# Optimization experiments

Hardware: AMD Instinct MI355X
Metric: run time of the kernel (lower is better)

Reference implementation:

```python
import jax, jax.numpy as jnp
import numpy as np

B, T, D, E, H, F, K = 4, 2048, 2048, 16, 1024, 1024, 2


def setup_inputs() -> dict:
    key = jax.random.key(0)
    ks = jax.random.split(key, 7)
    sD, sH, sF = D ** -0.5, H ** -0.5, F ** -0.5
    hidden_state = jax.random.normal(ks[0], (B, T, D), jnp.float32)
    Wr = jax.random.normal(ks[1], (D, E), jnp.float32) * sD      # router
    Wg = jax.random.normal(ks[2], (D, 1), jnp.float32) * sD      # shared gate
    W1 = jax.random.normal(ks[3], (E, D, H), jnp.float32) * sD   # expert up-proj
    W2 = jax.random.normal(ks[4], (E, H, D), jnp.float32) * sH   # expert down-proj
    W1s = jax.random.normal(ks[5], (D, F), jnp.float32) * sD     # shared expert up
    W2s = jax.random.normal(ks[6], (F, D), jnp.float32) * sF     # shared expert down
    return {"hidden_state": hidden_state, "Wr": Wr, "Wg": Wg,
            "W1": W1, "W2": W2, "W1s": W1s, "W2s": W2s}


def reference(hidden_state, Wr, Wg, W1, W2, W1s, W2s):
    b, t, d = hidden_state.shape
    N = b * t
    x = hidden_state.reshape(N, d)

    # Router: softmax scores + shared-expert sigmoid gate
    s = jax.nn.softmax(x @ Wr, axis=-1)           # [N, E]
    g_shared = jax.nn.sigmoid(x @ Wg)             # [N, 1]

    topk_vals, topk_idx = jax.lax.top_k(s, K)     # [N, K]

    # Dense combine weights: gate[n,e] = topk_vals if expert e chosen, else 0.
    # Mathematically identical to sort/gather/scatter-add dispatch in the source.
    gate = jnp.zeros((N, E), dtype=s.dtype).at[
        jnp.arange(N)[:, None], topk_idx].add(topk_vals)

    # Per-expert FFN (fixed small expert loop), gate-weighted combine
    y = jnp.zeros_like(x)
    for e in range(E):
        h = jax.nn.gelu(x @ W1[e], approximate=False)   # [N, H]
        y = y + gate[:, e:e + 1] * (h @ W2[e])

    # Shared expert, scaled by sigmoid gate
    shared = jax.nn.gelu(x @ W1s, approximate=False) @ W2s
    y = y + g_shared * shared
    y_out = y.reshape(b, t, d)

    # Aux stats (attention_mask is None branch)
    importance = s.mean(axis=0)                               # [E]
    counts = jnp.zeros((E,), jnp.float32).at[topk_idx.reshape(-1)].add(1.0)
    load = counts / (counts.sum() + 1e-12)
    return y_out, importance, load
```

## Files before the change

kernel.cpp:

```cpp
#include <hip/hip_runtime.h>
#include <hip/hip_bf16.h>


#define N_TOK 8192
#define DDIM  2048
#define NEXP  16
#define HDIM  1024
#define FDIM  1024
#define NASSIGN (N_TOK * 2)
#define NROWS (NASSIGN + N_TOK)

typedef __attribute__((ext_vector_type(8))) short bf16x8;
typedef __attribute__((ext_vector_type(4))) float f32x4;
typedef __attribute__((ext_vector_type(8))) unsigned short u16x8;
typedef __attribute__((ext_vector_type(4))) unsigned short u16x4;

__device__ inline unsigned short f2bf(float f) {
    unsigned int u = __builtin_bit_cast(unsigned int, f);
    u += 0x7FFFu + ((u >> 16) & 1u);
    return (unsigned short)(u >> 16);
}

__device__ inline float bf2f(unsigned short h) {
    return __builtin_bit_cast(float, (unsigned int)h << 16);
}

__device__ inline float gelu_f(float v) {
    return 0.5f * v * (1.0f + erff(v * 0.7071067811865475f));
}

__device__ inline void gld16(void* lds, const void* g) {
    __builtin_amdgcn_global_load_lds(
        (const __attribute__((address_space(1))) unsigned int*)g,
        (__attribute__((address_space(3))) unsigned int*)lds, 16, 0, 0);
}

__global__ __launch_bounds__(256) void zero_small(float* imp) {
    if (threadIdx.x < NEXP) imp[threadIdx.x] = 0.0f;
}

__global__ __launch_bounds__(256) void cast_x_kernel(const float* __restrict__ x,
                                                     unsigned short* __restrict__ xb) {
    size_t i = (size_t)blockIdx.x * 256 + threadIdx.x;
    const float4 a = ((const float4*)x)[i * 2];
    const float4 b = ((const float4*)x)[i * 2 + 1];
    u16x8 o;
    o[0] = f2bf(a.x); o[1] = f2bf(a.y); o[2] = f2bf(a.z); o[3] = f2bf(a.w);
    o[4] = f2bf(b.x); o[5] = f2bf(b.y); o[6] = f2bf(b.z); o[7] = f2bf(b.w);
    *(u16x8*)(xb + i * 8) = o;
}

template <int R, int C>
__global__ __launch_bounds__(256) void transpose_cast(const float* __restrict__ src,
                                                      unsigned short* __restrict__ dst) {
    __shared__ unsigned short t[64][66];
    const size_t zoff = (size_t)blockIdx.z * R * C;
    src += zoff; dst += zoff;
    const int r0 = blockIdx.y * 64, c0 = blockIdx.x * 64;
    const int tid = threadIdx.x;
    const int cr = tid >> 4;
    const int cc4 = (tid & 15) * 4;
#pragma unroll
    for (int it = 0; it < 4; ++it) {
        int row = cr + it * 16;
        const float4 v = *(const float4*)(src + (size_t)(r0 + row) * C + c0 + cc4);
        t[row][cc4 + 0] = f2bf(v.x); t[row][cc4 + 1] = f2bf(v.y);
        t[row][cc4 + 2] = f2bf(v.z); t[row][cc4 + 3] = f2bf(v.w);
    }
    __syncthreads();
#pragma unroll
    for (int it = 0; it < 4; ++it) {
        int cc = cr + it * 16;
        u16x4 o;
#pragma unroll
        for (int j = 0; j < 4; ++j) o[j] = t[cc4 + j][cc];
        *(u16x4*)(dst + (size_t)(c0 + cc) * R + r0 + cc4) = o;
    }
}

__global__ __launch_bounds__(256) void router_kernel(
    const float* __restrict__ x, const float* __restrict__ Wr, const float* __restrict__ Wg,
    float* __restrict__ gsh, int* __restrict__ t2i, float* __restrict__ t2v,
    float* __restrict__ imp) {
    __shared__ float simp[NEXP];
    const int tid = threadIdx.x, lane = tid & 63, w = tid >> 6;
    if (tid < NEXP) simp[tid] = 0.0f;
    __syncthreads();
    const int n = blockIdx.x * 4 + w;
    const float* xr = x + (size_t)n * DDIM;
    float acc[NEXP];
#pragma unroll
    for (int e = 0; e < NEXP; ++e) acc[e] = 0.0f;
    float ag = 0.0f;
    for (int j = 0; j < DDIM / 64; ++j) {
        int d = lane + j * 64;
        float xv = xr[d];
        const float* wr = Wr + (size_t)d * NEXP;
#pragma unroll
        for (int e = 0; e < NEXP; ++e) acc[e] = fmaf(xv, wr[e], acc[e]);
        ag = fmaf(xv, Wg[d], ag);
    }
#pragma unroll
    for (int off = 32; off; off >>= 1) {
#pragma unroll
        for (int e = 0; e < NEXP; ++e) acc[e] += __shfl_xor(acc[e], off);
        ag += __shfl_xor(ag, off);
    }
    if (lane == 0) {
        float mx = acc[0];
#pragma unroll
        for (int e = 1; e < NEXP; ++e) mx = fmaxf(mx, acc[e]);
        float p[NEXP], s = 0.0f;
#pragma unroll
        for (int e = 0; e < NEXP; ++e) { p[e] = expf(acc[e] - mx); s += p[e]; }
        const float inv = 1.0f / s;
        int i1 = 0; float v1 = -1.0f;
#pragma unroll
        for (int e = 0; e < NEXP; ++e) {
            p[e] *= inv;
            if (p[e] > v1) { v1 = p[e]; i1 = e; }
        }
        int i2 = 0; float v2 = -1.0f;
#pragma unroll
        for (int e = 0; e < NEXP; ++e) {
            if (e != i1 && p[e] > v2) { v2 = p[e]; i2 = e; }
        }
        t2i[2 * n] = i1; t2i[2 * n + 1] = i2;
        t2v[2 * n] = v1; t2v[2 * n + 1] = v2;
        gsh[n] = 1.0f / (1.0f + expf(-ag));
#pragma unroll
        for (int e = 0; e < NEXP; ++e) atomicAdd(&simp[e], p[e]);
    }
    __syncthreads();
    if (tid < NEXP) unsafeAtomicAdd(&imp[tid], simp[tid]);
}

__global__ __launch_bounds__(256) void scan_finalize(
    const int* __restrict__ t2i, const float* __restrict__ imp,
    int* __restrict__ offs, int* __restrict__ fill, float* __restrict__ out_tail) {
    __shared__ int hist[NEXP];
    const int tid = threadIdx.x;
    if (tid < NEXP) hist[tid] = 0;
    __syncthreads();
    for (int i = tid; i < NASSIGN; i += 256) atomicAdd(&hist[t2i[i]], 1);
    __syncthreads();
    if (tid == 0) {
        int o = 0;
        for (int e = 0; e < NEXP; ++e) { offs[e] = o; o += hist[e]; }
        offs[NEXP] = o;
        offs[NEXP + 1] = NROWS;
    }
    if (tid < NEXP) {
        fill[tid] = 0;
        out_tail[tid] = imp[tid] * (1.0f / (float)N_TOK);
        out_tail[NEXP + tid] = (float)hist[tid] / (float)NASSIGN;
    }
}

__global__ __launch_bounds__(256) void build_assign(
    const int* __restrict__ t2i, const float* __restrict__ t2v,
    const int* __restrict__ offs, int* __restrict__ fill,
    int* __restrict__ atok, float* __restrict__ agate, int* __restrict__ t2pos) {
    const int n = blockIdx.x * 256 + threadIdx.x;
#pragma unroll
    for (int k = 0; k < 2; ++k) {
        int e = t2i[2 * n + k];
        int pos = offs[e] + atomicAdd(&fill[e], 1);
        atok[pos] = n;
        agate[pos] = t2v[2 * n + k];
        t2pos[2 * n + k] = pos;
    }
    atok[NASSIGN + n] = n;
    agate[NASSIGN + n] = 1.0f;
}

__global__ __launch_bounds__(256) void combine_kernel(
    const unsigned short* __restrict__ contrib, const int* __restrict__ t2pos,
    const float* __restrict__ gsh, float* __restrict__ y) {
    const int gi = blockIdx.x * 256 + threadIdx.x;
    const int n = gi >> 8;
    const int d8 = (gi & 255) * 8;
    const int p0 = t2pos[2 * n], p1 = t2pos[2 * n + 1];
    const float g = gsh[n];
    u16x8 a = *(const u16x8*)(contrib + (size_t)p0 * DDIM + d8);
    u16x8 b = *(const u16x8*)(contrib + (size_t)p1 * DDIM + d8);
    u16x8 c = *(const u16x8*)(contrib + (size_t)(NASSIGN + n) * DDIM + d8);
    float4 y0, y1;
    y0.x = bf2f(a[0]) + bf2f(b[0]) + g * bf2f(c[0]);
    y0.y = bf2f(a[1]) + bf2f(b[1]) + g * bf2f(c[1]);
    y0.z = bf2f(a[2]) + bf2f(b[2]) + g * bf2f(c[2]);
    y0.w = bf2f(a[3]) + bf2f(b[3]) + g * bf2f(c[3]);
    y1.x = bf2f(a[4]) + bf2f(b[4]) + g * bf2f(c[4]);
    y1.y = bf2f(a[5]) + bf2f(b[5]) + g * bf2f(c[5]);
    y1.z = bf2f(a[6]) + bf2f(b[6]) + g * bf2f(c[6]);
    y1.w = bf2f(a[7]) + bf2f(b[7]) + g * bf2f(c[7]);
    float* yr = y + (size_t)n * DDIM + d8;
    *(float4*)yr = y0;
    *(float4*)(yr + 4) = y1;
}

template <int MODE>
__global__ __launch_bounds__(512, 2) void gemm2p(
    const unsigned short* __restrict__ A, const unsigned short* __restrict__ B,
    unsigned short* __restrict__ out,
    const int* __restrict__ offs, const int* __restrict__ atok,
    const float* __restrict__ agate) {
    constexpr int KD = MODE == 0 ? DDIM : HDIM;
    constexpr int NC = MODE == 0 ? HDIM : DDIM;
    const int e = blockIdx.z;
    const int m0 = offs[e];
    const int mE = offs[e + 1] - m0;
    const int tm = blockIdx.y;
    if (tm * 256 >= mE) return;
    const int n0 = blockIdx.x * 256;

    __shared__ __align__(16) unsigned short As_[2][256 * 32];
    __shared__ __align__(16) unsigned short Bs_[2][256 * 32];

    const int tid = threadIdx.x;
    const int lane = tid & 63, w = tid >> 6;
    const int wm = w >> 2, wn = w & 3;

    const unsigned short* sA[2];
    const unsigned short* sB[2];
    int dOff[2];
#pragma unroll
    for (int it = 0; it < 2; ++it) {
        int c = tid + it * 512;
        int row = c >> 2, slot = c & 3;
        int ksw = (slot ^ ((row >> 1) & 3)) * 8;
        int arow = tm * 256 + row; arow = arow < mE ? arow : mE - 1;
        if (MODE == 0)
            sA[it] = A + (size_t)atok[m0 + arow] * KD + ksw;
        else
            sA[it] = A + (size_t)(m0 + arow) * KD + ksw;
        sB[it] = B + (size_t)e * KD * NC + (size_t)(n0 + row) * KD + ksw;
        dOff[it] = c * 16;
    }

    f32x4 acc[8][4] = {};

    auto stage = [&](int b, int kk) {
        gld16((char*)As_[b] + dOff[0], sA[0] + kk);
        gld16((char*)As_[b] + dOff[1], sA[1] + kk);
        gld16((char*)Bs_[b] + dOff[0], sB[0] + kk);
        gld16((char*)Bs_[b] + dOff[1], sB[1] + kk);
    };
    auto compute = [&](int b) {
        const int c16 = lane & 15, q = lane >> 4;
        bf16x8 av[8], bv[4];
#pragma unroll
        for (int mi = 0; mi < 8; ++mi) {
            int r = wm * 128 + mi * 16 + c16;
            int s = q ^ ((r >> 1) & 3);
            av[mi] = *(const bf16x8*)((const char*)As_[b] + r * 64 + s * 16);
        }
#pragma unroll
        for (int ni = 0; ni < 4; ++ni) {
            int r = wn * 64 + ni * 16 + c16;
            int s = q ^ ((r >> 1) & 3);
            bv[ni] = *(const bf16x8*)((const char*)Bs_[b] + r * 64 + s * 16);
        }
#pragma unroll
        for (int mi = 0; mi < 8; ++mi)
#pragma unroll
            for (int ni = 0; ni < 4; ++ni)
                acc[mi][ni] = __builtin_amdgcn_mfma_f32_16x16x32_bf16(
                    av[mi], bv[ni], acc[mi][ni], 0, 0, 0);
    };

    stage(0, 0);
    __syncthreads();

#pragma unroll 1
    for (int kk = 0; kk < KD; kk += 64) {
        stage(1, kk + 32);
        compute(0);
        __syncthreads();
        if (kk + 64 < KD) stage(0, kk + 64);
        compute(1);
        __syncthreads();
    }

    const int col = lane & 15, r4 = (lane >> 4) * 4;
#pragma unroll
    for (int mi = 0; mi < 8; ++mi) {
#pragma unroll
        for (int r = 0; r < 4; ++r) {
            int grow = tm * 256 + wm * 128 + mi * 16 + r4 + r;
            if (grow >= mE) continue;
            float gate = (MODE == 0) ? agate[m0 + grow] : 0.0f;
#pragma unroll
            for (int ni = 0; ni < 4; ++ni) {
                int gcol = n0 + wn * 64 + ni * 16 + col;
                float v = acc[mi][ni][r];
                if (MODE == 0)
                    out[(size_t)(m0 + grow) * NC + gcol] = f2bf(gelu_f(v) * gate);
                else
                    out[(size_t)(m0 + grow) * NC + gcol] = f2bf(v);
            }
        }
    }
}

extern "C" void kernel_launch(void* const* d_in, const int* in_sizes, int n_in,
                              void* d_out, int out_size, void* d_ws, size_t ws_size,
                              hipStream_t stream) {
    const float* x   = (const float*)d_in[0];
    const float* Wr  = (const float*)d_in[1];
    const float* Wg  = (const float*)d_in[2];
    const float* W1  = (const float*)d_in[3];
    const float* W2  = (const float*)d_in[4];
    const float* W1s = (const float*)d_in[5];
    const float* W2s = (const float*)d_in[6];
    float* out = (float*)d_out;

    char* ws = (char*)d_ws;
    size_t off = 0;
    auto carve = [&](size_t bytes) { char* p = ws + off; off += (bytes + 255) & ~(size_t)255; return p; };
    unsigned short* xb    = (unsigned short*)carve((size_t)N_TOK * DDIM * 2);
    unsigned short* w1all = (unsigned short*)carve((size_t)(NEXP + 1) * DDIM * HDIM * 2);
    unsigned short* w2all = (unsigned short*)carve((size_t)(NEXP + 1) * HDIM * DDIM * 2);
    unsigned short* hb    = (unsigned short*)carve((size_t)NROWS * HDIM * 2);
    float* gsh            = (float*)carve((size_t)N_TOK * 4);
    int* t2i              = (int*)carve((size_t)N_TOK * 2 * 4);
    float* t2v            = (float*)carve((size_t)N_TOK * 2 * 4);
    int* atok             = (int*)carve((size_t)NROWS * 4);
    float* agate          = (float*)carve((size_t)NROWS * 4);
    int* t2pos            = (int*)carve((size_t)NASSIGN * 4);
    float* imp            = (float*)carve(256);
    int* offs             = (int*)carve(256);
    int* fill             = (int*)carve(256);
    if (ws_size < off) return;

    unsigned short* contrib = (unsigned short*)ws;

    float* out_tail = out + (size_t)N_TOK * DDIM;

    hipLaunchKernelGGL(zero_small, dim3(1), dim3(256), 0, stream, imp);
    hipLaunchKernelGGL(cast_x_kernel, dim3(N_TOK * DDIM / 8 / 256), dim3(256), 0, stream, x, xb);
    hipLaunchKernelGGL((transpose_cast<DDIM, HDIM>), dim3(HDIM / 64, DDIM / 64, NEXP), dim3(256), 0, stream, W1, w1all);
    hipLaunchKernelGGL((transpose_cast<DDIM, HDIM>), dim3(HDIM / 64, DDIM / 64, 1), dim3(256), 0, stream,
                       W1s, w1all + (size_t)NEXP * DDIM * HDIM);
    hipLaunchKernelGGL((transpose_cast<HDIM, DDIM>), dim3(DDIM / 64, HDIM / 64, NEXP), dim3(256), 0, stream, W2, w2all);
    hipLaunchKernelGGL((transpose_cast<HDIM, DDIM>), dim3(DDIM / 64, HDIM / 64, 1), dim3(256), 0, stream,
                       W2s, w2all + (size_t)NEXP * HDIM * DDIM);
    hipLaunchKernelGGL(router_kernel, dim3(N_TOK / 4), dim3(256), 0, stream, x, Wr, Wg, gsh, t2i, t2v, imp);
    hipLaunchKernelGGL(scan_finalize, dim3(1), dim3(256), 0, stream, t2i, imp, offs, fill, out_tail);
    hipLaunchKernelGGL(build_assign, dim3(N_TOK / 256), dim3(256), 0, stream, t2i, t2v, offs, fill, atok, agate, t2pos);

    hipLaunchKernelGGL((gemm2p<0>), dim3(HDIM / 256, N_TOK / 256, NEXP + 1), dim3(512), 0, stream,
                       xb, w1all, hb, offs, atok, agate);
    hipLaunchKernelGGL((gemm2p<1>), dim3(DDIM / 256, N_TOK / 256, NEXP + 1), dim3(512), 0, stream,
                       hb, w2all, contrib, offs, atok, agate);
    hipLaunchKernelGGL(combine_kernel, dim3(N_TOK * DDIM / 8 / 256), dim3(256), 0, stream,
                       contrib, t2pos, gsh, out);
}
```

Measured before the change: 750.1 us.

## Shrink grouped GEMM tiles to 128x128 and fold shared gate into first GEMM

Both grouped expert GEMMs move from 256x256 tiles with 512 threads to 128x128 tiles with 256 threads and four blocks per CU. The aim is to cut wasted work on partially filled per-expert row tiles and raise occupancy. The price is less data reuse per tile and more global loads. Separately, the shared-expert sigmoid gate is now written into agate, so the first GEMM epilogue applies it and the combine kernel no longer multiplies by it.

```diff
diff --git a/kernel.cpp b/kernel.cpp
--- a/kernel.cpp
+++ b/kernel.cpp
@@ -160,6 +160,7 @@
 __global__ __launch_bounds__(256) void build_assign(
     const int* __restrict__ t2i, const float* __restrict__ t2v,
     const int* __restrict__ offs, int* __restrict__ fill,
+    const float* __restrict__ gsh,
     int* __restrict__ atok, float* __restrict__ agate, int* __restrict__ t2pos) {
     const int n = blockIdx.x * 256 + threadIdx.x;
 #pragma unroll
@@ -171,36 +172,35 @@
         t2pos[2 * n + k] = pos;
     }
     atok[NASSIGN + n] = n;
-    agate[NASSIGN + n] = 1.0f;
+    agate[NASSIGN + n] = gsh[n];
 }
 
 __global__ __launch_bounds__(256) void combine_kernel(
     const unsigned short* __restrict__ contrib, const int* __restrict__ t2pos,
-    const float* __restrict__ gsh, float* __restrict__ y) {
+    float* __restrict__ y) {
     const int gi = blockIdx.x * 256 + threadIdx.x;
     const int n = gi >> 8;
     const int d8 = (gi & 255) * 8;
     const int p0 = t2pos[2 * n], p1 = t2pos[2 * n + 1];
-    const float g = gsh[n];
     u16x8 a = *(const u16x8*)(contrib + (size_t)p0 * DDIM + d8);
     u16x8 b = *(const u16x8*)(contrib + (size_t)p1 * DDIM + d8);
     u16x8 c = *(const u16x8*)(contrib + (size_t)(NASSIGN + n) * DDIM + d8);
     float4 y0, y1;
-    y0.x = bf2f(a[0]) + bf2f(b[0]) + g * bf2f(c[0]);
-    y0.y = bf2f(a[1]) + bf2f(b[1]) + g * bf2f(c[1]);
-    y0.z = bf2f(a[2]) + bf2f(b[2]) + g * bf2f(c[2]);
-    y0.w = bf2f(a[3]) + bf2f(b[3]) + g * bf2f(c[3]);
-    y1.x = bf2f(a[4]) + bf2f(b[4]) + g * bf2f(c[4]);
-    y1.y = bf2f(a[5]) + bf2f(b[5]) + g * bf2f(c[5]);
-    y1.z = bf2f(a[6]) + bf2f(b[6]) + g * bf2f(c[6]);
-    y1.w = bf2f(a[7]) + bf2f(b[7]) + g * bf2f(c[7]);
+    y0.x = bf2f(a[0]) + bf2f(b[0]) + bf2f(c[0]);
+    y0.y = bf2f(a[1]) + bf2f(b[1]) + bf2f(c[1]);
+    y0.z = bf2f(a[2]) + bf2f(b[2]) + bf2f(c[2]);
+    y0.w = bf2f(a[3]) + bf2f(b[3]) + bf2f(c[3]);
+    y1.x = bf2f(a[4]) + bf2f(b[4]) + bf2f(c[4]);
+    y1.y = bf2f(a[5]) + bf2f(b[5]) + bf2f(c[5]);
+    y1.z = bf2f(a[6]) + bf2f(b[6]) + bf2f(c[6]);
+    y1.w = bf2f(a[7]) + bf2f(b[7]) + bf2f(c[7]);
     float* yr = y + (size_t)n * DDIM + d8;
     *(float4*)yr = y0;
     *(float4*)(yr + 4) = y1;
 }
 
 template <int MODE>
-__global__ __launch_bounds__(512, 2) void gemm2p(
+__global__ __launch_bounds__(256, 4) void gemm128(
     const unsigned short* __restrict__ A, const unsigned short* __restrict__ B,
     unsigned short* __restrict__ out,
     const int* __restrict__ offs, const int* __restrict__ atok,
@@ -211,25 +211,24 @@
     const int m0 = offs[e];
     const int mE = offs[e + 1] - m0;
     const int tm = blockIdx.y;
-    if (tm * 256 >= mE) return;
-    const int n0 = blockIdx.x * 256;
-
-    __shared__ __align__(16) unsigned short As_[2][256 * 32];
-    __shared__ __align__(16) unsigned short Bs_[2][256 * 32];
-
-    const int tid = threadIdx.x;
-    const int lane = tid & 63, w = tid >> 6;
-    const int wm = w >> 2, wn = w & 3;
+    if (tm * 128 >= mE) return;
+    const int n0 = blockIdx.x * 128;
+
+    __shared__ __align__(16) unsigned short As_[2][128 * 32];
+    __shared__ __align__(16) unsigned short Bs_[2][128 * 32];
+
+    const int tid = threadIdx.x, lane = tid & 63;
+    const int wid = tid >> 6, wm = wid >> 1, wn = wid & 1;
 
     const unsigned short* sA[2];
     const unsigned short* sB[2];
     int dOff[2];
 #pragma unroll
     for (int it = 0; it < 2; ++it) {
-        int c = tid + it * 512;
+        int c = tid + it * 256;
         int row = c >> 2, slot = c & 3;
         int ksw = (slot ^ ((row >> 1) & 3)) * 8;
-        int arow = tm * 256 + row; arow = arow < mE ? arow : mE - 1;
+        int arow = tm * 128 + row; arow = arow < mE ? arow : mE - 1;
         if (MODE == 0)
             sA[it] = A + (size_t)atok[m0 + arow] * KD + ksw;
         else
@@ -238,7 +237,7 @@
         dOff[it] = c * 16;
     }
 
-    f32x4 acc[8][4] = {};
+    f32x4 acc[4][4] = {};
 
     auto stage = [&](int b, int kk) {
         gld16((char*)As_[b] + dOff[0], sA[0] + kk);
@@ -248,10 +247,10 @@
     };
     auto compute = [&](int b) {
         const int c16 = lane & 15, q = lane >> 4;
-        bf16x8 av[8], bv[4];
-#pragma unroll
-        for (int mi = 0; mi < 8; ++mi) {
-            int r = wm * 128 + mi * 16 + c16;
+        bf16x8 av[4], bv[4];
+#pragma unroll
+        for (int mi = 0; mi < 4; ++mi) {
+            int r = wm * 64 + mi * 16 + c16;
             int s = q ^ ((r >> 1) & 3);
             av[mi] = *(const bf16x8*)((const char*)As_[b] + r * 64 + s * 16);
         }
@@ -262,7 +261,7 @@
             bv[ni] = *(const bf16x8*)((const char*)Bs_[b] + r * 64 + s * 16);
         }
 #pragma unroll
-        for (int mi = 0; mi < 8; ++mi)
+        for (int mi = 0; mi < 4; ++mi)
 #pragma unroll
             for (int ni = 0; ni < 4; ++ni)
                 acc[mi][ni] = __builtin_amdgcn_mfma_f32_16x16x32_bf16(
@@ -284,10 +283,10 @@
 
     const int col = lane & 15, r4 = (lane >> 4) * 4;
 #pragma unroll
-    for (int mi = 0; mi < 8; ++mi) {
+    for (int mi = 0; mi < 4; ++mi) {
 #pragma unroll
         for (int r = 0; r < 4; ++r) {
-            int grow = tm * 256 + wm * 128 + mi * 16 + r4 + r;
+            int grow = tm * 128 + wm * 64 + mi * 16 + r4 + r;
             if (grow >= mE) continue;
             float gate = (MODE == 0) ? agate[m0 + grow] : 0.0f;
 #pragma unroll
@@ -347,12 +346,12 @@
                        W2s, w2all + (size_t)NEXP * HDIM * DDIM);
     hipLaunchKernelGGL(router_kernel, dim3(N_TOK / 4), dim3(256), 0, stream, x, Wr, Wg, gsh, t2i, t2v, imp);
     hipLaunchKernelGGL(scan_finalize, dim3(1), dim3(256), 0, stream, t2i, imp, offs, fill, out_tail);
-    hipLaunchKernelGGL(build_assign, dim3(N_TOK / 256), dim3(256), 0, stream, t2i, t2v, offs, fill, atok, agate, t2pos);
-
-    hipLaunchKernelGGL((gemm2p<0>), dim3(HDIM / 256, N_TOK / 256, NEXP + 1), dim3(512), 0, stream,
+    hipLaunchKernelGGL(build_assign, dim3(N_TOK / 256), dim3(256), 0, stream, t2i, t2v, offs, fill, gsh, atok, agate, t2pos);
+
+    hipLaunchKernelGGL((gemm128<0>), dim3(HDIM / 128, N_TOK / 128, NEXP + 1), dim3(256), 0, stream,
                        xb, w1all, hb, offs, atok, agate);
-    hipLaunchKernelGGL((gemm2p<1>), dim3(DDIM / 256, N_TOK / 256, NEXP + 1), dim3(512), 0, stream,
+    hipLaunchKernelGGL((gemm128<1>), dim3(DDIM / 128, N_TOK / 128, NEXP + 1), dim3(256), 0, stream,
                        hb, w2all, contrib, offs, atok, agate);
     hipLaunchKernelGGL(combine_kernel, dim3(N_TOK * DDIM / 8 / 256), dim3(256), 0, stream,
-                       contrib, t2pos, gsh, out);
-}
+                       contrib, t2pos, out);
+}
```

Measured after the change: 614.6 us. 1.22x faster.
